# Performance work log

Measured on AMD Instinct MI355X. Metric: run time of the kernel, lower is better.

## Reference

```python
import jax, jax.numpy as jnp
import numpy as np

B, K, F, C = 256, 16, 128, 2
EPS = 1e-5


def setup_inputs() -> dict:
    key = jax.random.key(0)
    ks = jax.random.split(key, 16)
    n = lambda k, shape, s=1.0: (jax.random.normal(k, shape, dtype=jnp.float32) * s)
    return {
        "x0": n(ks[0], (B, F)),
        "x1": n(ks[1], (B, K, F)),
        "x2": n(ks[2], (B, K * K, F)),
        "x3": n(ks[3], (B, K ** 3, F)),
        "W0": n(ks[4], (2 * F, F), 0.05), "b0": n(ks[5], (F,), 0.05),
        "W1": n(ks[6], (2 * F, F), 0.05), "b1": n(ks[7], (F,), 0.05),
        "W2": n(ks[8], (2 * F, F), 0.05), "b2": n(ks[9], (F,), 0.05),
        "lin1_W": n(ks[10], (F, 8), 0.05), "lin1_b": n(ks[11], (8,), 0.05),
        "bn_gamma": jnp.ones((8,), jnp.float32), "bn_beta": jnp.zeros((8,), jnp.float32),
        "lin2_W": n(ks[12], (8, C), 0.05), "lin2_b": n(ks[13], (C,), 0.05),
    }


def _agg_mean(x):
    # block-wise mean over groups of K along dim 1: [B, N, F] -> [B, N//K, F]
    b, n_, f = x.shape
    return x.reshape(b, n_ // K, K, f).mean(axis=2)


def reference(x0, x1, x2, x3, W0, b0, W1, b1, W2, b2,
              lin1_W, lin1_b, bn_gamma, bn_beta, lin2_W, lin2_b):
    # layer i=3: mean-agg x3 blocks, concat with x2, Linear(2F->F)+ReLU
    h2 = jax.nn.relu(jnp.concatenate([_agg_mean(x3), x2], axis=2) @ W2 + b2)
    # layer i=2
    h1 = jax.nn.relu(jnp.concatenate([_agg_mean(h2), x1], axis=2) @ W1 + b1)
    # layer i=1: agg gives [B,1,F]; squeeze and concat along feature dim
    h0 = jax.nn.relu(jnp.concatenate([_agg_mean(h1)[:, 0, :], x0], axis=1) @ W0 + b0)
    # classifier head: Linear -> BatchNorm1d (training batch stats) -> Linear -> Sigmoid
    z = h0 @ lin1_W + lin1_b                       # [B, 8]
    mu = z.mean(axis=0)
    var = jnp.mean(jnp.square(z - mu), axis=0)     # biased var, as torch BN
    zn = (z - mu) * jax.lax.rsqrt(var + EPS) * bn_gamma + bn_beta
    return jax.nn.sigmoid(zn @ lin2_W + lin2_b)    # [B, C]
```

## Files before the change

kernel.cpp:

```cpp
#include <hip/hip_runtime.h>
#include <math.h>

#define NTHR 256

typedef __bf16 bf16x8 __attribute__((ext_vector_type(8)));
typedef float  f32x4  __attribute__((ext_vector_type(4)));
typedef float  f32x4v __attribute__((ext_vector_type(4)));

__device__ __forceinline__ unsigned short f2bf(float x) {
    unsigned int u = __float_as_uint(x);
    return (unsigned short)((u + 0x7fffu + ((u >> 16) & 1u)) >> 16);
}
__device__ __forceinline__ ushort4 pack4v(f32x4v v) {
    return make_ushort4(f2bf(v[0]), f2bf(v[1]), f2bf(v[2]), f2bf(v[3]));
}
__device__ __forceinline__ f32x4v ntload4(const float* p) {
    return __builtin_nontemporal_load((const f32x4v*)p);
}

template<int TM, bool AGG_IN, bool AGG_OUT>
__global__ __launch_bounds__(NTHR, 4)
void layer_kernel(const float* __restrict__ deep,
                  const float* __restrict__ shal,
                  const float* __restrict__ W,
                  const float* __restrict__ bias,
                  float* __restrict__ outp)
{
    constexpr int MT = TM / 16;
    __shared__ unsigned short A[TM][264];
    const int t  = threadIdx.x;
    const int m0 = blockIdx.x * TM;

    {
        const int r8 = t >> 5;
        const int l  = t & 31;
        const int fo = l * 4;
        for (int rr = r8; rr < TM; rr += 8) {
            const int m = m0 + rr;
            f32x4v s, sh;
            if (AGG_IN) {
                const float* dp = deep + (size_t)m * 2048 + fo;
                s = ntload4(dp);
                #pragma unroll
                for (int k = 1; k < 16; ++k) s += ntload4(dp + k * 128);
                s *= (1.0f / 16.0f);
                sh = ntload4(shal + (size_t)m * 128 + fo);
            } else {
                s  = *(const f32x4v*)(deep + (size_t)m * 128 + fo);
                sh = *(const f32x4v*)(shal + (size_t)m * 128 + fo);
            }
            *(ushort4*)&A[rr][fo]       = pack4v(s);
            *(ushort4*)&A[rr][128 + fo] = pack4v(sh);
        }
    }

    const int l    = t & 63;
    const int w    = t >> 6;
    const int lo16 = l & 15;
    const int q    = l >> 4;
    const int c0   = w * 32;

    bf16x8 Bf[16];
    #pragma unroll
    for (int kt = 0; kt < 8; ++kt) {
        #pragma unroll
        for (int nt = 0; nt < 2; ++nt) {
            const float* p = W + (size_t)(kt * 32 + q * 8) * 128 + c0 + nt * 16 + lo16;
            union { unsigned short u[8]; bf16x8 v; } tmp;
            #pragma unroll
            for (int j = 0; j < 8; ++j) tmp.u[j] = f2bf(p[(size_t)j * 128]);
            Bf[kt * 2 + nt] = tmp.v;
        }
    }
    __syncthreads();

    f32x4 acc[MT][2];
    #pragma unroll
    for (int mt = 0; mt < MT; ++mt) {
        acc[mt][0] = (f32x4){0.f, 0.f, 0.f, 0.f};
        acc[mt][1] = (f32x4){0.f, 0.f, 0.f, 0.f};
    }
    #pragma unroll
    for (int kt = 0; kt < 8; ++kt) {
        #pragma unroll
        for (int mt = 0; mt < MT; ++mt) {
            bf16x8 Af = *(const bf16x8*)&A[mt * 16 + lo16][kt * 32 + q * 8];
            acc[mt][0] = __builtin_amdgcn_mfma_f32_16x16x32_bf16(Af, Bf[kt * 2 + 0], acc[mt][0], 0, 0, 0);
            acc[mt][1] = __builtin_amdgcn_mfma_f32_16x16x32_bf16(Af, Bf[kt * 2 + 1], acc[mt][1], 0, 0, 0);
        }
    }

    const float bn0 = bias[c0 + lo16];
    const float bn1 = bias[c0 + 16 + lo16];
    if (AGG_OUT) {
        #pragma unroll
        for (int mt = 0; mt < MT; ++mt) {
            float v0 = 0.f, v1 = 0.f;
            #pragma unroll
            for (int r = 0; r < 4; ++r) {
                v0 += fmaxf(acc[mt][0][r] + bn0, 0.0f);
                v1 += fmaxf(acc[mt][1][r] + bn1, 0.0f);
            }
            v0 += __shfl_xor(v0, 16, 64); v0 += __shfl_xor(v0, 32, 64);
            v1 += __shfl_xor(v1, 16, 64); v1 += __shfl_xor(v1, 32, 64);
            const int g = blockIdx.x * MT + mt;
            if (q == 0) outp[(size_t)g * 128 + c0 + lo16]      = v0 * 0.0625f;
            if (q == 1) outp[(size_t)g * 128 + c0 + 16 + lo16] = v1 * 0.0625f;
        }
    } else {
        #pragma unroll
        for (int mt = 0; mt < MT; ++mt) {
            #pragma unroll
            for (int r = 0; r < 4; ++r) {
                const int row = m0 + mt * 16 + q * 4 + r;
                float* op = outp + (size_t)row * 128;
                op[c0 + lo16]      = fmaxf(acc[mt][0][r] + bn0, 0.0f);
                op[c0 + 16 + lo16] = fmaxf(acc[mt][1][r] + bn1, 0.0f);
            }
        }
    }
}

__global__ __launch_bounds__(NTHR)
void head_kernel(const float* __restrict__ h0,
                 const float* __restrict__ l1W,
                 const float* __restrict__ l1b,
                 const float* __restrict__ gamma,
                 const float* __restrict__ beta,
                 const float* __restrict__ l2W,
                 const float* __restrict__ l2b,
                 float* __restrict__ out)
{
    __shared__ float z[256][8];
    __shared__ float w1s[128 * 8];
    __shared__ float ps[32][8];
    __shared__ float pq[32][8];
    __shared__ float scale_s[8], shift_s[8];

    const int t  = threadIdx.x;
    const int j  = t & 7;
    const int rg = t >> 3;

    #pragma unroll
    for (int i = 0; i < 4; ++i) w1s[t * 4 + i] = l1W[t * 4 + i];
    __syncthreads();

    const float bj = l1b[j];
    for (int it = 0; it < 8; ++it) {
        const int b = it * 32 + rg;
        const float4* hr = (const float4*)(h0 + (size_t)b * 128);
        float s = bj;
        #pragma unroll
        for (int f4 = 0; f4 < 32; ++f4) {
            float4 h = hr[f4];
            s += h.x * w1s[(f4 * 4 + 0) * 8 + j];
            s += h.y * w1s[(f4 * 4 + 1) * 8 + j];
            s += h.z * w1s[(f4 * 4 + 2) * 8 + j];
            s += h.w * w1s[(f4 * 4 + 3) * 8 + j];
        }
        z[b][j] = s;
    }
    __syncthreads();

    {
        float s = 0.0f, qq = 0.0f;
        #pragma unroll
        for (int r = 0; r < 8; ++r) {
            float v = z[rg * 8 + r][j];
            s += v; qq += v * v;
        }
        ps[rg][j] = s; pq[rg][j] = qq;
    }
    __syncthreads();

    if (t < 8) {
        float s = 0.0f, qq = 0.0f;
        #pragma unroll
        for (int p = 0; p < 32; ++p) { s += ps[p][t]; qq += pq[p][t]; }
        const float mu  = s * (1.0f / 256.0f);
        const float var = qq * (1.0f / 256.0f) - mu * mu;
        const float sc  = gamma[t] * rsqrtf(var + 1e-5f);
        scale_s[t] = sc;
        shift_s[t] = beta[t] - mu * sc;
    }
    __syncthreads();

    {
        float o0 = l2b[0], o1 = l2b[1];
        #pragma unroll
        for (int jj = 0; jj < 8; ++jj) {
            const float zn = z[t][jj] * scale_s[jj] + shift_s[jj];
            o0 += zn * l2W[jj * 2 + 0];
            o1 += zn * l2W[jj * 2 + 1];
        }
        out[t * 2 + 0] = 1.0f / (1.0f + expf(-o0));
        out[t * 2 + 1] = 1.0f / (1.0f + expf(-o1));
    }
}

extern "C" void kernel_launch(void* const* d_in, const int* in_sizes, int n_in,
                              void* d_out, int out_size, void* d_ws, size_t ws_size,
                              hipStream_t stream)
{
    const float* x0    = (const float*)d_in[0];
    const float* x1    = (const float*)d_in[1];
    const float* x2    = (const float*)d_in[2];
    const float* x3    = (const float*)d_in[3];
    const float* W0    = (const float*)d_in[4];
    const float* b0    = (const float*)d_in[5];
    const float* W1    = (const float*)d_in[6];
    const float* b1    = (const float*)d_in[7];
    const float* W2    = (const float*)d_in[8];
    const float* b2    = (const float*)d_in[9];
    const float* l1W   = (const float*)d_in[10];
    const float* l1b   = (const float*)d_in[11];
    const float* gamma = (const float*)d_in[12];
    const float* beta  = (const float*)d_in[13];
    const float* l2W   = (const float*)d_in[14];
    const float* l2b   = (const float*)d_in[15];
    float* out = (float*)d_out;

    float* h2m = (float*)d_ws;
    float* h1m = h2m + (size_t)4096 * 128;
    float* h0  = h1m + (size_t)256 * 128;

    hipLaunchKernelGGL((layer_kernel<64, true, true>), dim3(65536 / 64), dim3(NTHR), 0, stream,
                       x3, x2, W2, b2, h2m);
    hipLaunchKernelGGL((layer_kernel<64, false, true>), dim3(4096 / 64), dim3(NTHR), 0, stream,
                       h2m, x1, W1, b1, h1m);
    hipLaunchKernelGGL((layer_kernel<64, false, false>), dim3(256 / 64), dim3(NTHR), 0, stream,
                       h1m, x0, W0, b0, h0);
    hipLaunchKernelGGL(head_kernel, dim3(1), dim3(NTHR), 0, stream,
                       h0, l1W, l1b, gamma, beta, l2W, l2b, out);
}
```

Before: 731.3 us.

## Fuse layer 2 into layer 3 kernel and merge final layer with head

```diff
diff --git a/kernel.cpp b/kernel.cpp
--- a/kernel.cpp
+++ b/kernel.cpp
@@ -5,62 +5,21 @@
 
 typedef __bf16 bf16x8 __attribute__((ext_vector_type(8)));
 typedef float  f32x4  __attribute__((ext_vector_type(4)));
-typedef float  f32x4v __attribute__((ext_vector_type(4)));
 
 __device__ __forceinline__ unsigned short f2bf(float x) {
     unsigned int u = __float_as_uint(x);
     return (unsigned short)((u + 0x7fffu + ((u >> 16) & 1u)) >> 16);
 }
-__device__ __forceinline__ ushort4 pack4v(f32x4v v) {
+__device__ __forceinline__ ushort4 pack4v(f32x4 v) {
     return make_ushort4(f2bf(v[0]), f2bf(v[1]), f2bf(v[2]), f2bf(v[3]));
 }
-__device__ __forceinline__ f32x4v ntload4(const float* p) {
-    return __builtin_nontemporal_load((const f32x4v*)p);
-}
-
-template<int TM, bool AGG_IN, bool AGG_OUT>
-__global__ __launch_bounds__(NTHR, 4)
-void layer_kernel(const float* __restrict__ deep,
-                  const float* __restrict__ shal,
-                  const float* __restrict__ W,
-                  const float* __restrict__ bias,
-                  float* __restrict__ outp)
-{
-    constexpr int MT = TM / 16;
-    __shared__ unsigned short A[TM][264];
-    const int t  = threadIdx.x;
-    const int m0 = blockIdx.x * TM;
-
-    {
-        const int r8 = t >> 5;
-        const int l  = t & 31;
-        const int fo = l * 4;
-        for (int rr = r8; rr < TM; rr += 8) {
-            const int m = m0 + rr;
-            f32x4v s, sh;
-            if (AGG_IN) {
-                const float* dp = deep + (size_t)m * 2048 + fo;
-                s = ntload4(dp);
-                #pragma unroll
-                for (int k = 1; k < 16; ++k) s += ntload4(dp + k * 128);
-                s *= (1.0f / 16.0f);
-                sh = ntload4(shal + (size_t)m * 128 + fo);
-            } else {
-                s  = *(const f32x4v*)(deep + (size_t)m * 128 + fo);
-                sh = *(const f32x4v*)(shal + (size_t)m * 128 + fo);
-            }
-            *(ushort4*)&A[rr][fo]       = pack4v(s);
-            *(ushort4*)&A[rr][128 + fo] = pack4v(sh);
-        }
-    }
-
-    const int l    = t & 63;
-    const int w    = t >> 6;
-    const int lo16 = l & 15;
-    const int q    = l >> 4;
-    const int c0   = w * 32;
-
-    bf16x8 Bf[16];
+__device__ __forceinline__ f32x4 ntload4(const float* p) {
+    return __builtin_nontemporal_load((const f32x4*)p);
+}
+
+__device__ __forceinline__ void load_bfrags(const float* __restrict__ W,
+                                            int c0, int q, int lo16, bf16x8* Bf)
+{
     #pragma unroll
     for (int kt = 0; kt < 8; ++kt) {
         #pragma unroll
@@ -72,111 +31,208 @@
             Bf[kt * 2 + nt] = tmp.v;
         }
     }
-    __syncthreads();
-
-    f32x4 acc[MT][2];
-    #pragma unroll
-    for (int mt = 0; mt < MT; ++mt) {
+}
+
+__global__ __launch_bounds__(NTHR, 4)
+void k1_kernel(const float* __restrict__ x3,
+               const float* __restrict__ x2,
+               const float* __restrict__ x1,
+               const float* __restrict__ W2,
+               const float* __restrict__ b2,
+               const float* __restrict__ W1,
+               const float* __restrict__ b1,
+               float* __restrict__ h1)
+{
+    __shared__ unsigned short A[64][264];
+    const int t  = threadIdx.x;
+    const int m0 = blockIdx.x * 64;
+
+    {
+        const int r8 = t >> 5;
+        const int fo = (t & 31) * 4;
+        for (int rr = r8; rr < 64; rr += 8) {
+            const int m = m0 + rr;
+            const float* dp = x3 + (size_t)m * 2048 + fo;
+            f32x4 s = ntload4(dp);
+            #pragma unroll
+            for (int k = 1; k < 16; ++k) s += ntload4(dp + k * 128);
+            s *= (1.0f / 16.0f);
+            f32x4 sh = ntload4(x2 + (size_t)m * 128 + fo);
+            *(ushort4*)&A[rr][fo]       = pack4v(s);
+            *(ushort4*)&A[rr][128 + fo] = pack4v(sh);
+        }
+    }
+
+    const int l    = t & 63;
+    const int w    = t >> 6;
+    const int lo16 = l & 15;
+    const int q    = l >> 4;
+    const int c0   = w * 32;
+
+    bf16x8 Bf[16];
+    load_bfrags(W2, c0, q, lo16, Bf);
+    __syncthreads();
+
+    f32x4 acc[4][2];
+    #pragma unroll
+    for (int mt = 0; mt < 4; ++mt) {
         acc[mt][0] = (f32x4){0.f, 0.f, 0.f, 0.f};
         acc[mt][1] = (f32x4){0.f, 0.f, 0.f, 0.f};
     }
     #pragma unroll
     for (int kt = 0; kt < 8; ++kt) {
         #pragma unroll
-        for (int mt = 0; mt < MT; ++mt) {
+        for (int mt = 0; mt < 4; ++mt) {
             bf16x8 Af = *(const bf16x8*)&A[mt * 16 + lo16][kt * 32 + q * 8];
             acc[mt][0] = __builtin_amdgcn_mfma_f32_16x16x32_bf16(Af, Bf[kt * 2 + 0], acc[mt][0], 0, 0, 0);
             acc[mt][1] = __builtin_amdgcn_mfma_f32_16x16x32_bf16(Af, Bf[kt * 2 + 1], acc[mt][1], 0, 0, 0);
         }
     }
 
-    const float bn0 = bias[c0 + lo16];
-    const float bn1 = bias[c0 + 16 + lo16];
-    if (AGG_OUT) {
-        #pragma unroll
-        for (int mt = 0; mt < MT; ++mt) {
-            float v0 = 0.f, v1 = 0.f;
+    const float bn0 = b2[c0 + lo16];
+    const float bn1 = b2[c0 + 16 + lo16];
+    __syncthreads();
+    #pragma unroll
+    for (int mt = 0; mt < 4; ++mt) {
+        float v0 = 0.f, v1 = 0.f;
+        #pragma unroll
+        for (int r = 0; r < 4; ++r) {
+            v0 += fmaxf(acc[mt][0][r] + bn0, 0.0f);
+            v1 += fmaxf(acc[mt][1][r] + bn1, 0.0f);
+        }
+        v0 += __shfl_xor(v0, 16, 64); v0 += __shfl_xor(v0, 32, 64);
+        v1 += __shfl_xor(v1, 16, 64); v1 += __shfl_xor(v1, 32, 64);
+        if (q == 0) *(unsigned short*)&A[mt][c0 + lo16]      = f2bf(v0 * 0.0625f);
+        if (q == 1) *(unsigned short*)&A[mt][c0 + 16 + lo16] = f2bf(v1 * 0.0625f);
+    }
+    if (l < 32) {
+        f32x4 sh = ntload4(x1 + (size_t)(blockIdx.x * 4 + w) * 128 + l * 4);
+        *(ushort4*)&A[w][128 + l * 4] = pack4v(sh);
+    }
+    load_bfrags(W1, c0, q, lo16, Bf);
+    __syncthreads();
+
+    f32x4 a20 = (f32x4){0.f, 0.f, 0.f, 0.f};
+    f32x4 a21 = (f32x4){0.f, 0.f, 0.f, 0.f};
+    #pragma unroll
+    for (int kt = 0; kt < 8; ++kt) {
+        bf16x8 Af = *(const bf16x8*)&A[lo16][kt * 32 + q * 8];
+        a20 = __builtin_amdgcn_mfma_f32_16x16x32_bf16(Af, Bf[kt * 2 + 0], a20, 0, 0, 0);
+        a21 = __builtin_amdgcn_mfma_f32_16x16x32_bf16(Af, Bf[kt * 2 + 1], a21, 0, 0, 0);
+    }
+    if (q == 0) {
+        const float c1a = b1[c0 + lo16];
+        const float c1b = b1[c0 + 16 + lo16];
+        float* hp = h1 + (size_t)(blockIdx.x * 4) * 128;
+        #pragma unroll
+        for (int r = 0; r < 4; ++r) {
+            hp[r * 128 + c0 + lo16]      = fmaxf(a20[r] + c1a, 0.0f);
+            hp[r * 128 + c0 + 16 + lo16] = fmaxf(a21[r] + c1b, 0.0f);
+        }
+    }
+}
+
+__global__ __launch_bounds__(NTHR)
+void k2_kernel(const float* __restrict__ h1,
+               const float* __restrict__ x0,
+               const float* __restrict__ W0,
+               const float* __restrict__ b0,
+               const float* __restrict__ l1W,
+               const float* __restrict__ l1b,
+               float* __restrict__ z_ws,
+               float* __restrict__ part)
+{
+    __shared__ unsigned short A[16][264];
+    __shared__ float zh[16][132];
+    __shared__ float w1s[128 * 8];
+    __shared__ float zs[16][9];
+    const int t  = threadIdx.x;
+    const int m0 = blockIdx.x * 16;
+
+    {
+        const int r8 = t >> 5;
+        const int fo = (t & 31) * 4;
+        #pragma unroll
+        for (int rr = r8; rr < 16; rr += 8) {
+            const int m = m0 + rr;
+            const float* dp = h1 + (size_t)m * 2048 + fo;
+            f32x4 s = *(const f32x4*)dp;
             #pragma unroll
-            for (int r = 0; r < 4; ++r) {
-                v0 += fmaxf(acc[mt][0][r] + bn0, 0.0f);
-                v1 += fmaxf(acc[mt][1][r] + bn1, 0.0f);
-            }
-            v0 += __shfl_xor(v0, 16, 64); v0 += __shfl_xor(v0, 32, 64);
-            v1 += __shfl_xor(v1, 16, 64); v1 += __shfl_xor(v1, 32, 64);
-            const int g = blockIdx.x * MT + mt;
-            if (q == 0) outp[(size_t)g * 128 + c0 + lo16]      = v0 * 0.0625f;
-            if (q == 1) outp[(size_t)g * 128 + c0 + 16 + lo16] = v1 * 0.0625f;
-        }
-    } else {
-        #pragma unroll
-        for (int mt = 0; mt < MT; ++mt) {
-            #pragma unroll
-            for (int r = 0; r < 4; ++r) {
-                const int row = m0 + mt * 16 + q * 4 + r;
-                float* op = outp + (size_t)row * 128;
-                op[c0 + lo16]      = fmaxf(acc[mt][0][r] + bn0, 0.0f);
-                op[c0 + 16 + lo16] = fmaxf(acc[mt][1][r] + bn1, 0.0f);
-            }
-        }
+            for (int k = 1; k < 16; ++k) s += *(const f32x4*)(dp + k * 128);
+            s *= (1.0f / 16.0f);
+            f32x4 sh = *(const f32x4*)(x0 + (size_t)m * 128 + fo);
+            *(ushort4*)&A[rr][fo]       = pack4v(s);
+            *(ushort4*)&A[rr][128 + fo] = pack4v(sh);
+        }
+    }
+    *(f32x4*)&w1s[t * 4] = *(const f32x4*)&l1W[t * 4];
+
+    const int l    = t & 63;
+    const int w    = t >> 6;
+    const int lo16 = l & 15;
+    const int q    = l >> 4;
+    const int c0   = w * 32;
+
+    bf16x8 Bf[16];
+    load_bfrags(W0, c0, q, lo16, Bf);
+    __syncthreads();
+
+    f32x4 a0 = (f32x4){0.f, 0.f, 0.f, 0.f};
+    f32x4 a1 = (f32x4){0.f, 0.f, 0.f, 0.f};
+    #pragma unroll
+    for (int kt = 0; kt < 8; ++kt) {
+        bf16x8 Af = *(const bf16x8*)&A[lo16][kt * 32 + q * 8];
+        a0 = __builtin_amdgcn_mfma_f32_16x16x32_bf16(Af, Bf[kt * 2 + 0], a0, 0, 0, 0);
+        a1 = __builtin_amdgcn_mfma_f32_16x16x32_bf16(Af, Bf[kt * 2 + 1], a1, 0, 0, 0);
+    }
+    const float bb0 = b0[c0 + lo16];
+    const float bb1 = b0[c0 + 16 + lo16];
+    #pragma unroll
+    for (int r = 0; r < 4; ++r) {
+        zh[q * 4 + r][c0 + lo16]      = fmaxf(a0[r] + bb0, 0.0f);
+        zh[q * 4 + r][c0 + 16 + lo16] = fmaxf(a1[r] + bb1, 0.0f);
+    }
+    __syncthreads();
+
+    if (t < 128) {
+        const int m = t >> 3, j = t & 7;
+        float s = l1b[j];
+        #pragma unroll
+        for (int c = 0; c < 128; ++c) s += zh[m][c] * w1s[c * 8 + j];
+        z_ws[(size_t)(m0 + m) * 8 + j] = s;
+        zs[m][j] = s;
+    }
+    __syncthreads();
+    if (t < 8) {
+        float s = 0.f, qq = 0.f;
+        #pragma unroll
+        for (int m = 0; m < 16; ++m) { const float v = zs[m][t]; s += v; qq += v * v; }
+        part[blockIdx.x * 8 + t]       = s;
+        part[128 + blockIdx.x * 8 + t] = qq;
     }
 }
 
 __global__ __launch_bounds__(NTHR)
-void head_kernel(const float* __restrict__ h0,
-                 const float* __restrict__ l1W,
-                 const float* __restrict__ l1b,
-                 const float* __restrict__ gamma,
-                 const float* __restrict__ beta,
-                 const float* __restrict__ l2W,
-                 const float* __restrict__ l2b,
-                 float* __restrict__ out)
-{
-    __shared__ float z[256][8];
-    __shared__ float w1s[128 * 8];
-    __shared__ float ps[32][8];
-    __shared__ float pq[32][8];
+void k3_kernel(const float* __restrict__ part,
+               const float* __restrict__ z_ws,
+               const float* __restrict__ gamma,
+               const float* __restrict__ beta,
+               const float* __restrict__ l2W,
+               const float* __restrict__ l2b,
+               float* __restrict__ out)
+{
     __shared__ float scale_s[8], shift_s[8];
-
-    const int t  = threadIdx.x;
-    const int j  = t & 7;
-    const int rg = t >> 3;
-
-    #pragma unroll
-    for (int i = 0; i < 4; ++i) w1s[t * 4 + i] = l1W[t * 4 + i];
-    __syncthreads();
-
-    const float bj = l1b[j];
-    for (int it = 0; it < 8; ++it) {
-        const int b = it * 32 + rg;
-        const float4* hr = (const float4*)(h0 + (size_t)b * 128);
-        float s = bj;
-        #pragma unroll
-        for (int f4 = 0; f4 < 32; ++f4) {
-            float4 h = hr[f4];
-            s += h.x * w1s[(f4 * 4 + 0) * 8 + j];
-            s += h.y * w1s[(f4 * 4 + 1) * 8 + j];
-            s += h.z * w1s[(f4 * 4 + 2) * 8 + j];
-            s += h.w * w1s[(f4 * 4 + 3) * 8 + j];
-        }
-        z[b][j] = s;
-    }
-    __syncthreads();
-
-    {
-        float s = 0.0f, qq = 0.0f;
-        #pragma unroll
-        for (int r = 0; r < 8; ++r) {
-            float v = z[rg * 8 + r][j];
-            s += v; qq += v * v;
-        }
-        ps[rg][j] = s; pq[rg][j] = qq;
-    }
-    __syncthreads();
-
+    __shared__ float w2s[16], b2s[2];
+    const int t = threadIdx.x;
+    if (t < 16) w2s[t] = l2W[t];
+    if (t < 2)  b2s[t] = l2b[t];
     if (t < 8) {
-        float s = 0.0f, qq = 0.0f;
-        #pragma unroll
-        for (int p = 0; p < 32; ++p) { s += ps[p][t]; qq += pq[p][t]; }
+        float s = 0.f, qq = 0.f;
+        #pragma unroll
+        for (int p = 0; p < 16; ++p) {
+            s  += part[p * 8 + t];
+            qq += part[128 + p * 8 + t];
+        }
         const float mu  = s * (1.0f / 256.0f);
         const float var = qq * (1.0f / 256.0f) - mu * mu;
         const float sc  = gamma[t] * rsqrtf(var + 1e-5f);
@@ -184,18 +240,16 @@
         shift_s[t] = beta[t] - mu * sc;
     }
     __syncthreads();
-
-    {
-        float o0 = l2b[0], o1 = l2b[1];
-        #pragma unroll
-        for (int jj = 0; jj < 8; ++jj) {
-            const float zn = z[t][jj] * scale_s[jj] + shift_s[jj];
-            o0 += zn * l2W[jj * 2 + 0];
-            o1 += zn * l2W[jj * 2 + 1];
-        }
-        out[t * 2 + 0] = 1.0f / (1.0f + expf(-o0));
-        out[t * 2 + 1] = 1.0f / (1.0f + expf(-o1));
-    }
+    float o0 = b2s[0], o1 = b2s[1];
+    const float* zr = z_ws + (size_t)t * 8;
+    #pragma unroll
+    for (int j = 0; j < 8; ++j) {
+        const float zn = zr[j] * scale_s[j] + shift_s[j];
+        o0 += zn * w2s[j * 2 + 0];
+        o1 += zn * w2s[j * 2 + 1];
+    }
+    out[t * 2 + 0] = 1.0f / (1.0f + expf(-o0));
+    out[t * 2 + 1] = 1.0f / (1.0f + expf(-o1));
 }
 
 extern "C" void kernel_launch(void* const* d_in, const int* in_sizes, int n_in,
@@ -220,16 +274,14 @@
     const float* l2b   = (const float*)d_in[15];
     float* out = (float*)d_out;
 
-    float* h2m = (float*)d_ws;
-    float* h1m = h2m + (size_t)4096 * 128;
-    float* h0  = h1m + (size_t)256 * 128;
-
-    hipLaunchKernelGGL((layer_kernel<64, true, true>), dim3(65536 / 64), dim3(NTHR), 0, stream,
-                       x3, x2, W2, b2, h2m);
-    hipLaunchKernelGGL((layer_kernel<64, false, true>), dim3(4096 / 64), dim3(NTHR), 0, stream,
-                       h2m, x1, W1, b1, h1m);
-    hipLaunchKernelGGL((layer_kernel<64, false, false>), dim3(256 / 64), dim3(NTHR), 0, stream,
-                       h1m, x0, W0, b0, h0);
-    hipLaunchKernelGGL(head_kernel, dim3(1), dim3(NTHR), 0, stream,
-                       h0, l1W, l1b, gamma, beta, l2W, l2b, out);
-}
+    float* h1   = (float*)d_ws;
+    float* z_ws = h1 + (size_t)4096 * 128;
+    float* part = z_ws + (size_t)256 * 8;
+
+    hipLaunchKernelGGL(k1_kernel, dim3(65536 / 64), dim3(NTHR), 0, stream,
+                       x3, x2, x1, W2, b2, W1, b1, h1);
+    hipLaunchKernelGGL(k2_kernel, dim3(16), dim3(NTHR), 0, stream,
+                       h1, x0, W0, b0, l1W, l1b, z_ws, part);
+    hipLaunchKernelGGL(k3_kernel, dim3(1), dim3(NTHR), 0, stream,
+                       part, z_ws, gamma, beta, l2W, l2b, out);
+}
```

Measured after the change: 723.7 us. Within noise of the previous version (-1.0%).
